# Kernel tuning notes

Measured on AMD Instinct MI355X. Metric: run time of the kernel, lower is better.

## Reference

```python
import jax, jax.numpy as jnp
import numpy as np

D_EMBED = 384
D_FF = 64
TAU = 0.1
T0, T1 = 0.0, 1.0
N_STEPS = 10


def setup_inputs() -> dict:
    key = jax.random.key(0)
    ks = jax.random.split(key, 6)
    B, n, d, f = 64, 1024, D_EMBED, D_FF
    init = lambda k, sh, fan: (jax.random.normal(k, sh, jnp.float32) / np.sqrt(fan)).astype(jnp.float32)
    return {
        "embeddings": jax.random.normal(ks[0], (B, n, d), jnp.float32),
        "W1": init(ks[1], (d + 1, f), d + 1), "b1": jnp.zeros((f,), jnp.float32),
        "W2": init(ks[2], (f, f), f),       "b2": jnp.zeros((f,), jnp.float32),
        "W3": init(ks[3], (f, d), f),       "b3": jnp.zeros((d,), jnp.float32),
        "Ws": init(ks[4], (d, 1), d),       "bs": jnp.zeros((1,), jnp.float32),
    }


def reference(embeddings, W1, b1, W2, b2, W3, b3, Ws, bs):
    B, n, d = embeddings.shape
    h0 = embeddings.reshape(B * n, d)
    dt = (T1 - T0) / N_STEPS

    def ode_f(t, h):
        # time-aware dynamics: concat scalar t to hidden state
        t_col = jnp.full((h.shape[0], 1), t, dtype=h.dtype)
        x = jnp.concatenate([h, t_col], axis=-1)
        x = jnp.tanh(x @ W1 + b1)
        x = jnp.tanh(x @ W2 + b2)
        return x @ W3 + b3

    def rk4_step(h, t):
        k1 = ode_f(t, h)
        k2 = ode_f(t + dt * 0.5, h + (dt * 0.5) * k1)
        k3 = ode_f(t + dt * 0.5, h + (dt * 0.5) * k2)
        k4 = ode_f(t + dt, h + dt * k3)
        return h + (dt / 6.0) * (k1 + 2.0 * k2 + 2.0 * k3 + k4), None

    ts = T0 + dt * jnp.arange(N_STEPS, dtype=jnp.float32)
    h_final, _ = jax.lax.scan(rk4_step, h0, ts)
    h_final = h_final.reshape(B, n, d)

    scores = (h_final @ Ws + bs).squeeze(-1)  # (B, n)

    # NeuralSort (Grover et al.): P_hat = softmax((C - A@1@1^T)^T / tau)
    s_col = scores[:, :, None]                        # (B, n, 1)
    A = jnp.abs(s_col - scores[:, None, :])           # (B, n, n) pairwise |s_i - s_j|
    row_sum = jnp.sum(A, axis=-1, keepdims=True)      # A @ one one^T, broadcast over cols
    scaling = (n + 1 - 2.0 * (jnp.arange(n, dtype=scores.dtype) + 1.0))  # (n,)
    C = s_col * scaling[None, None, :]                # C[b,i,j] = s_i * scaling_j
    P_max = jnp.transpose(C - row_sum, (0, 2, 1))
    P_hat = jax.nn.softmax(P_max / TAU, axis=-1)      # (B, n, n) soft permutation

    x_sorted = jnp.einsum('bij,bjd->bid', P_hat, embeddings)
    return x_sorted, scores
```

## Files before the change

kernel.cpp:

```cpp
#include <hip/hip_runtime.h>
#include <hip/hip_bf16.h>

#define NT 1024
#define DD 384
#define FF 64

typedef __attribute__((ext_vector_type(8))) _Float16 half8;
typedef __attribute__((ext_vector_type(4))) float f32x4;
typedef __attribute__((ext_vector_type(4))) unsigned uint32x4;

#define LO_SCALE 2048.f
#define INV2048  4.8828125e-4f

__device__ __forceinline__ float tanh_fast(float x){
    x = fminf(fmaxf(x, -15.f), 15.f);
    float e = __expf(2.f*x);
    return (e - 1.f) * __builtin_amdgcn_rcpf(e + 1.f);
}

__device__ __forceinline__ unsigned short h2u(_Float16 h){ return __builtin_bit_cast(unsigned short, h); }

__device__ __forceinline__ unsigned short split2_comp(float x, int comp){
    _Float16 hi = (_Float16)x;
    if (comp == 0) return h2u(hi);
    float r = (x - (float)hi) * LO_SCALE;
    _Float16 lo = (_Float16)r;
    return h2u(lo);
}

__device__ __forceinline__ void split_pack4(const float* v, unsigned* ph, unsigned* pl){
#pragma unroll
    for (int p=0;p<2;++p){
        float a=v[2*p], b=v[2*p+1];
        _Float16 ha=(_Float16)a, hb=(_Float16)b;
        ph[p] = (unsigned)h2u(ha) | ((unsigned)h2u(hb)<<16);
        float ra=(a-(float)ha)*LO_SCALE, rb=(b-(float)hb)*LO_SCALE;
        pl[p] = __builtin_bit_cast(unsigned, __builtin_amdgcn_cvt_pkrtz(ra, rb));
    }
}

__global__ void k_prep(const float* __restrict__ W1, const float* __restrict__ W2,
                       const float* __restrict__ W3, unsigned short* __restrict__ F)
{
    unsigned short* W1F = F;
    unsigned short* W2F = F + 49152;
    unsigned short* W3F = F + 57344;
    const int t = blockIdx.x*256 + threadIdx.x;
    const int NTH = gridDim.x*256;
    for (int i=t; i<49152; i+=NTH){
        int j=i&7, l=(i>>3)&63, u=i>>9;
        int kb=u%12, v=u/12, mb=v&3, comp=v>>2;
        int k=kb*32+8*(l>>4)+j, c=mb*16+(l&15);
        W1F[i] = split2_comp(W1[k*64+c], comp);
    }
    for (int i=t; i<8192; i+=NTH){
        int j=i&7, l=(i>>3)&63, u=i>>9;
        int kb=u&1, v=u>>1, mb=v&3, comp=v>>2;
        int k=kb*32+8*(l>>4)+j, c=mb*16+(l&15);
        W2F[i] = split2_comp(W2[k*64+c], comp);
    }
    for (int i=t; i<49152; i+=NTH){
        int j=i&7, l=(i>>3)&63, u=i>>9;
        int kb=u&1, v=u>>1, mb=v%24, comp=v/24;
        int k=kb*32+8*(l>>4)+j, c=mb*16+(l&15);
        W3F[i] = split2_comp(W3[k*384+c], comp);
    }
}

__global__ void k_prepE(const float* __restrict__ emb, unsigned short* __restrict__ EF)
{
    __shared__ float tile[32][388];
    const int b   = blockIdx.x >> 5;
    const int kb  = blockIdx.x & 31;
    const int tid = threadIdx.x;
    const float* src = emb + ((long long)b*NT + kb*32)*DD;
    for (int o = tid; o < 32*96; o += 256){
        int r = o/96, c4 = (o%96)*4;
        *(float4*)&tile[r][c4] = *(const float4*)&src[r*384 + c4];
    }
    __syncthreads();
    unsigned short* dst = EF + ((long long)b*24*32 + kb)*512;
    for (int o = tid; o < 24*512; o += 256){
        int mb = o >> 9, q = o & 511;
        int l = q >> 3, jj = q & 7;
        float v = tile[8*(l>>4)+jj][mb*16 + (l&15)];
        dst[(long long)mb*16384 + q] = h2u((_Float16)v);
    }
}

#define MFMA3(AH,AL,BH,BL,ACC,ACC2) do{ \
    ACC  = __builtin_amdgcn_mfma_f32_16x16x32_f16(AH,BH,ACC,0,0,0); \
    ACC2 = __builtin_amdgcn_mfma_f32_16x16x32_f16(AH,BL,ACC2,0,0,0); \
    ACC2 = __builtin_amdgcn_mfma_f32_16x16x32_f16(AL,BH,ACC2,0,0,0); \
}while(0)

struct AF { half8 h, l; };
#define LDA(P, CS) AF{ *(const half8*)(P), *(const half8*)((P)+(CS)) }
#define LDB(BASE, KB) do{ \
    bh = *(const half8*)((BASE) + (KB)*2048); \
    bl = *(const half8*)((BASE) + (KB)*2048 + 1024); \
}while(0)

__global__ __launch_bounds__(512) __attribute__((amdgpu_waves_per_eu(2,2)))
void k_ode(const float* __restrict__ emb,
           const float* __restrict__ W1,
           const float* __restrict__ b1, const float* __restrict__ b2,
           const float* __restrict__ b3, const float* __restrict__ Ws,
           const float* __restrict__ bs,
           const unsigned short* __restrict__ W1F,
           const unsigned short* __restrict__ W2F,
           const unsigned short* __restrict__ W3F,
           float* __restrict__ scores)
{
    extern __shared__ char smem[];
    unsigned short* hf  = (unsigned short*)smem;
    unsigned short* x1f = hf  + 24576;
    unsigned short* x2f = x1f + 4096;
    unsigned short* w1h = x2f + 4096;
    float*          h0l = (float*)(smem + 114688);

    unsigned* hf32  = (unsigned*)hf;
    unsigned* x1f32 = (unsigned*)x1f;
    unsigned* x2f32 = (unsigned*)x2f;

    const int tid  = threadIdx.x;
    const int lane = tid & 63;
    const int w    = __builtin_amdgcn_readfirstlane(tid >> 6);
    const int g    = lane >> 4;
    const int rr   = lane & 15;
    const int nb   = w & 1;
    const int mbA  = w >> 1;
    const int rowl = nb*16 + rr;
    const long long row0 = (long long)blockIdx.x * 32;
    const float dt = 0.1f;

    {
        const unsigned* srcw = (const unsigned*)W1F;
        unsigned* dstw = (unsigned*)w1h;
        for (int o = tid; o < 12288; o += 512) dstw[o] = srcw[o];
    }

    const unsigned short* hrd  = hf  + nb*512 + lane*8;
    const unsigned short* x1rd = x1f + nb*512 + lane*8;
    const unsigned short* x2rd = x2f + nb*512 + lane*8;
    const unsigned wxp = nb*256 + rr*4 + 2*(g&1);
    const unsigned wx1 = ((unsigned)(mbA>>1))*1024 + 64u*((2*mbA+(g>>1))&3) + wxp;
    const int h0base = rowl*324 + mbA*80 + 4*g;
    float h0r5[4];

    float arc[24];
#pragma unroll
    for (int t=0;t<6;++t){
        f32x4 v = *(const f32x4*)(emb + (row0+rowl)*DD + mbA*96 + t*16 + 4*g);
        float hw[4] = {v[0],v[1],v[2],v[3]};
        if (t < 5) *(float4*)(h0l + h0base + 16*t) = make_float4(hw[0],hw[1],hw[2],hw[3]);
        else {
#pragma unroll
            for (int r=0;r<4;++r) h0r5[r] = hw[r];
        }
        unsigned ph[2],pl[2];
        split_pack4(hw,ph,pl);
        const unsigned wh = ((unsigned)((6*mbA+t)>>1))*1024 + 64u*((2*t+(g>>1))&3) + wxp;
        *(uint2*)(hf32 + wh       ) = make_uint2(ph[0],ph[1]);
        *(uint2*)(hf32 + wh +  512) = make_uint2(pl[0],pl[1]);
    }

#define M3SEC(T, ACC, ACC2) do{ \
    ACC = *(const f32x4*)(b3 + mbA*96 + 16*(T) + 4*g); \
    ACC2 = (f32x4){0.f,0.f,0.f,0.f}; \
    const unsigned short* A3 = W3F + (unsigned)((6*mbA+(T))*2)*512 + lane*8; \
    AF w0 = LDA(A3, 24576); \
    AF w1 = LDA(A3+512, 24576); \
    MFMA3(w0.h,w0.l,B0h,B0l,ACC,ACC2); \
    MFMA3(w1.h,w1.l,B1h,B1l,ACC,ACC2); \
    __builtin_amdgcn_sched_barrier(0); \
}while(0)

#define M3UPD(T, ACC, ACC2) do{ \
    float h0v[4]; \
    if ((T) < 5){ \
        f32x4 _hv = *(const f32x4*)(h0l + h0base + 16*(T)); \
        h0v[0]=_hv[0]; h0v[1]=_hv[1]; h0v[2]=_hv[2]; h0v[3]=_hv[3]; \
    } else { \
        _Pragma("unroll") \
        for (int r=0;r<4;++r) h0v[r] = h0r5[r]; \
    } \
    float hw[4]; \
    if (stage < 3){ \
        _Pragma("unroll") \
        for (int r=0;r<4;++r){ float kr=fmaf(ACC2[r], INV2048, ACC[r]); \
            arc[4*(T)+r] = fmaf(wacc, kr, arc[4*(T)+r]); \
            hw[r] = fmaf(cs, kr, h0v[r]); } \
    } else { \
        _Pragma("unroll") \
        for (int r=0;r<4;++r){ float kr=fmaf(ACC2[r], INV2048, ACC[r]); \
            arc[4*(T)+r] = fmaf(wacc, kr, arc[4*(T)+r]); \
            hw[r] = h0v[r] + arc[4*(T)+r]; } \
        if ((T) < 5) *(float4*)(h0l + h0base + 16*(T)) = make_float4(hw[0],hw[1],hw[2],hw[3]); \
        else { \
            _Pragma("unroll") \
            for (int r=0;r<4;++r) h0r5[r] = hw[r]; \
        } \
    } \
    unsigned ph[2],pl[2]; \
    split_pack4(hw,ph,pl); \
    const unsigned wh = ((unsigned)((6*mbA+(T))>>1))*1024 + 64u*((2*(T)+(g>>1))&3) + wxp; \
    *(uint2*)(hf32 + wh       ) = make_uint2(ph[0],ph[1]); \
    *(uint2*)(hf32 + wh +  512) = make_uint2(pl[0],pl[1]); \
}while(0)

#pragma unroll 1
    for (int step=0; step<10; ++step){
        const float tstep = dt*(float)step;
#pragma unroll
        for (int j=0;j<24;++j) arc[j]=0.f;

#pragma unroll 1
        for (int stage=0; stage<4; ++stage){
            const float ts = tstep + ((stage==0)?0.f:((stage==3)?dt:0.5f*dt));
            __syncthreads();

            f32x4 accA, accB, accLA, accLB;
            {
                f32x4 b1v = *(const f32x4*)(b1 + mbA*16 + 4*g);
                f32x4 wtv = *(const f32x4*)(W1 + 384*64 + mbA*16 + 4*g);
#pragma unroll
                for (int r=0;r<4;++r){ accA[r] = fmaf(ts, wtv[r], b1v[r]); accB[r] = 0.f; accLA[r] = 0.f; accLB[r] = 0.f; }
            }
            {
                const unsigned short* H1 = w1h + mbA*6144 + lane*8;
                const unsigned short* L1 = W1F + 24576 + mbA*6144 + lane*8;
                half8 l0 = *(const half8*)(L1);
                half8 l1 = *(const half8*)(L1 + 512);
#pragma unroll 1
                for (int p=0;p<6;++p){
                    half8 hh0 = *(const half8*)(H1 + (2*p)*512);
                    half8 hh1 = *(const half8*)(H1 + (2*p+1)*512);
                    const int kb2 = (p<5) ? (2*p+2) : 0;
                    half8 nl0 = *(const half8*)(L1 + kb2*512);
                    half8 nl1 = *(const half8*)(L1 + (kb2+1)*512);
                    half8 bh,bl;
                    LDB(hrd, 2*p);
                    MFMA3(hh0,l0,bh,bl,accA,accLA);
                    LDB(hrd, 2*p+1);
                    MFMA3(hh1,l1,bh,bl,accB,accLB);
                    l0 = nl0; l1 = nl1;
                }
            }
            {
                float xv[4];
#pragma unroll
                for (int r=0;r<4;++r) xv[r] = tanh_fast(accA[r] + accB[r] + (accLA[r]+accLB[r])*INV2048);
                unsigned ph[2],pl[2];
                split_pack4(xv,ph,pl);
                *(uint2*)(x1f32 + wx1       ) = make_uint2(ph[0],ph[1]);
                *(uint2*)(x1f32 + wx1 +  512) = make_uint2(pl[0],pl[1]);
            }
            __syncthreads();

            f32x4 acc2 = *(const f32x4*)(b2 + mbA*16 + 4*g);
            f32x4 acc2L;
            {
#pragma unroll
                for (int r=0;r<4;++r) acc2L[r] = 0.f;
                const unsigned short* A2 = W2F + mbA*1024 + lane*8;
                AF c0 = LDA(A2, 4096);
                AF c1 = LDA(A2 + 512, 4096);
                half8 bh,bl;
                LDB(x1rd, 0);
                MFMA3(c0.h,c0.l,bh,bl,acc2,acc2L);
                LDB(x1rd, 1);
                MFMA3(c1.h,c1.l,bh,bl,acc2,acc2L);
            }
            {
                float xv[4];
#pragma unroll
                for (int r=0;r<4;++r) xv[r] = tanh_fast(acc2[r] + acc2L[r]*INV2048);
                unsigned ph[2],pl[2];
                split_pack4(xv,ph,pl);
                *(uint2*)(x2f32 + wx1       ) = make_uint2(ph[0],ph[1]);
                *(uint2*)(x2f32 + wx1 +  512) = make_uint2(pl[0],pl[1]);
            }
            __syncthreads();

            const float wacc = (dt/6.f)*((stage==1||stage==2)?2.f:1.f);
            const float cs   = (stage==2)?dt:0.5f*dt;
            {
                half8 B0h = *(const half8*)(x2rd);
                half8 B0l = *(const half8*)(x2rd + 1024);
                half8 B1h = *(const half8*)(x2rd + 2048);
                half8 B1l = *(const half8*)(x2rd + 3072);
                f32x4 ac0,ac1,ac2b,ac3,ac4,ac5;
                f32x4 c0,c1,c2,c3,c4,c5;
                M3SEC(0, ac0, c0);
                M3SEC(1, ac1, c1);   M3UPD(0, ac0, c0);
                M3SEC(2, ac2b, c2);  M3UPD(1, ac1, c1);
                M3SEC(3, ac3, c3);   M3UPD(2, ac2b, c2);
                M3SEC(4, ac4, c4);   M3UPD(3, ac3, c3);
                M3SEC(5, ac5, c5);   M3UPD(4, ac4, c4);
                M3UPD(5, ac5, c5);
            }
        }
    }

    float part = 0.f;
#pragma unroll
    for (int t=0;t<6;++t){
        float hv[4];
        if (t < 5){
            f32x4 _hv = *(const f32x4*)(h0l + h0base + 16*t);
            hv[0]=_hv[0]; hv[1]=_hv[1]; hv[2]=_hv[2]; hv[3]=_hv[3];
        } else {
#pragma unroll
            for (int r=0;r<4;++r) hv[r] = h0r5[r];
        }
        f32x4 wsv = *(const f32x4*)(Ws + mbA*96 + t*16 + 4*g);
#pragma unroll
        for (int r=0;r<4;++r) part = fmaf(hv[r], wsv[r], part);
    }
    __syncthreads();
    float* red = (float*)x1f;
    red[rowl*16 + mbA*4 + g] = part;
    __syncthreads();
    if (tid < 32){
        float s = bs[0];
#pragma unroll
        for (int q=0;q<16;++q) s += red[tid*16+q];
        scores[row0 + tid] = s;
    }
#undef M3SEC
#undef M3UPD
}

__global__ void k_rowsum(const float* __restrict__ scores, float* __restrict__ rs)
{
    __shared__ float s[NT];
    const int b   = blockIdx.x >> 2;
    const int q   = blockIdx.x & 3;
    const int tid = threadIdx.x;
    for (int i=tid; i<NT; i+=256) s[i] = scores[b*NT + i];
    __syncthreads();
    const int i = q*256 + tid;
    const float si = s[i];
    float sum = 0.f;
#pragma unroll 8
    for (int j=0; j<NT; ++j) sum += fabsf(si - s[j]);
    rs[b*NT + i] = sum;
}

__global__ __launch_bounds__(512)
void k_pvm(const unsigned short* __restrict__ EF, const float* __restrict__ scores,
           const float* __restrict__ rs, float* __restrict__ out)
{
    __shared__ float s_tr[2*NT];
    __shared__ float red_m[16][33];
    __shared__ float red_s[16][33];
    __shared__ float s_MI[64];

    const int tid = threadIdx.x;
    const int b   = blockIdx.x >> 5;
    const int j0  = (blockIdx.x & 31) * 32;
    const float invT2 = 10.f * 1.44269504f;

    for (int i = tid; i < NT; i += 512){
        s_tr[2*i  ] =  scores[b*NT + i] * invT2;
        s_tr[2*i+1] = -rs[b*NT + i] * invT2;
    }
    __syncthreads();

    {
        const int jl = tid & 31;
        const int ch = tid >> 5;
        const float SC = 1023.f - 2.f*(float)(j0 + jl);
        const int ib = ch*64;
        float m = -3.0e38f;
#pragma unroll 4
        for (int i = ib; i < ib+64; ++i)
            m = fmaxf(m, fmaf(s_tr[2*i], SC, s_tr[2*i+1]));
        float sum = 0.f;
#pragma unroll 4
        for (int i = ib; i < ib+64; ++i)
            sum += exp2f(fmaf(s_tr[2*i], SC, s_tr[2*i+1]) - m);
        red_m[ch][jl] = m; red_s[ch][jl] = sum;
    }
    __syncthreads();
    if (tid < 32){
        float M = -3.0e38f;
#pragma unroll
        for (int c=0;c<16;++c) M = fmaxf(M, red_m[c][tid]);
        float S = 0.f;
#pragma unroll
        for (int c=0;c<16;++c) S += red_s[c][tid] * exp2f(red_m[c][tid] - M);
        s_MI[tid]    = M;
        s_MI[32+tid] = __builtin_amdgcn_rcpf(S);
    }
    __syncthreads();

    const int lane = tid & 63;
    const int w    = __builtin_amdgcn_readfirstlane(tid >> 6);
    const int g    = lane >> 4;
    const int rr   = lane & 15;
    const int nb   = w & 1;
    const int mbA  = w >> 1;
    const int jl   = nb*16 + rr;
    const float SCv = 1023.f - 2.f*(float)(j0 + jl);
    const float Mv  = s_MI[jl];
    const float Iv  = s_MI[32 + jl];

    f32x4 ac0={0,0,0,0}, ac1={0,0,0,0}, ac2={0,0,0,0},
          ac3={0,0,0,0}, ac4={0,0,0,0}, ac5={0,0,0,0};

    const unsigned short* Abase = EF + (((long long)b*24 + mbA*6)*32)*512 + lane*8;

#pragma unroll 2
    for (int kb = 0; kb < 32; ++kb){
        const float* str = s_tr + 2*(kb*32 + 8*g);
        uint32x4 pw;
#pragma unroll
        for (int p=0;p<4;++p){
            float L0 = fmaf(str[4*p  ], SCv, str[4*p+1]) - Mv;
            float L1 = fmaf(str[4*p+2], SCv, str[4*p+3]) - Mv;
            pw[p] = __builtin_bit_cast(unsigned,
                        __builtin_amdgcn_cvt_pkrtz(exp2f(L0), exp2f(L1)));
        }
        half8 Pf = __builtin_bit_cast(half8, pw);
        const unsigned short* A = Abase + kb*512;
        ac0 = __builtin_amdgcn_mfma_f32_16x16x32_f16(*(const half8*)(A          ), Pf, ac0, 0,0,0);
        ac1 = __builtin_amdgcn_mfma_f32_16x16x32_f16(*(const half8*)(A + 16384  ), Pf, ac1, 0,0,0);
        ac2 = __builtin_amdgcn_mfma_f32_16x16x32_f16(*(const half8*)(A + 2*16384), Pf, ac2, 0,0,0);
        ac3 = __builtin_amdgcn_mfma_f32_16x16x32_f16(*(const half8*)(A + 3*16384), Pf, ac3, 0,0,0);
        ac4 = __builtin_amdgcn_mfma_f32_16x16x32_f16(*(const half8*)(A + 4*16384), Pf, ac4, 0,0,0);
        ac5 = __builtin_amdgcn_mfma_f32_16x16x32_f16(*(const half8*)(A + 5*16384), Pf, ac5, 0,0,0);
    }

    float* op = out + ((long long)b*NT + j0 + jl)*DD + mbA*96 + 4*g;
    *(float4*)(op       ) = make_float4(ac0[0]*Iv, ac0[1]*Iv, ac0[2]*Iv, ac0[3]*Iv);
    *(float4*)(op + 16  ) = make_float4(ac1[0]*Iv, ac1[1]*Iv, ac1[2]*Iv, ac1[3]*Iv);
    *(float4*)(op + 32  ) = make_float4(ac2[0]*Iv, ac2[1]*Iv, ac2[2]*Iv, ac2[3]*Iv);
    *(float4*)(op + 48  ) = make_float4(ac3[0]*Iv, ac3[1]*Iv, ac3[2]*Iv, ac3[3]*Iv);
    *(float4*)(op + 64  ) = make_float4(ac4[0]*Iv, ac4[1]*Iv, ac4[2]*Iv, ac4[3]*Iv);
    *(float4*)(op + 80  ) = make_float4(ac5[0]*Iv, ac5[1]*Iv, ac5[2]*Iv, ac5[3]*Iv);
}

__global__ __launch_bounds__(256, 2)
void k_pv(const float* __restrict__ emb, const float* __restrict__ scores,
          const float* __restrict__ rs, float* __restrict__ out)
{
    __shared__ float s_tt[NT];
    __shared__ float s_rp[NT];
    __shared__ float red_m[8][33];
    __shared__ float red_s[8][33];
    __shared__ float s_M[32], s_I[32];

    const int tid = threadIdx.x;
    const int b   = blockIdx.x >> 5;
    const int j0  = (blockIdx.x & 31) * 32;
    const float invT = 10.f;

    for (int i=tid; i<NT; i+=256){
        s_tt[i] =  scores[b*NT + i] * invT;
        s_rp[i] = -rs[b*NT + i] * invT;
    }
    __syncthreads();
    {
        const int jl = tid & 31;
        const int ch = tid >> 5;
        const float SC = 1023.f - 2.f*(float)(j0 + jl);
        const int ibeg = ch*128;
        float m = -3.0e38f;
#pragma unroll 4
        for (int i=ibeg; i<ibeg+128; ++i){
            float L = fmaf(s_tt[i], SC, s_rp[i]);
            m = fmaxf(m, L);
        }
        float sum = 0.f;
#pragma unroll 4
        for (int i=ibeg; i<ibeg+128; ++i){
            float L = fmaf(s_tt[i], SC, s_rp[i]);
            sum += __expf(L - m);
        }
        red_m[ch][jl] = m; red_s[ch][jl] = sum;
    }
    __syncthreads();
    if (tid < 32){
        float M = -3.0e38f;
#pragma unroll
        for (int c=0; c<8; ++c) M = fmaxf(M, red_m[c][tid]);
        float S = 0.f;
#pragma unroll
        for (int c=0; c<8; ++c) S += red_s[c][tid]*__expf(red_m[c][tid]-M);
        s_M[tid] = M;
        s_I[tid] = 1.f/S;
    }
    __syncthreads();

    const int tx = tid & 31;
    const int jy = tid >> 5;
    float accv[4][12];
#pragma unroll
    for (int v=0; v<4; ++v)
#pragma unroll
        for (int u=0; u<12; ++u) accv[v][u] = 0.f;

    float SCv[4], Mv[4], Iv[4];
#pragma unroll
    for (int v=0; v<4; ++v){
        const int jl = jy + 8*v;
        SCv[v] = 1023.f - 2.f*(float)(j0 + jl);
        Mv[v]  = s_M[jl];
        Iv[v]  = s_I[jl];
    }
    const float* ep = emb + ((long long)b*NT)*DD + tx;
#pragma unroll 2
    for (int i=0; i<NT; ++i){
        const float ti = s_tt[i], ri = s_rp[i];
        float ev[12];
#pragma unroll
        for (int u=0; u<12; ++u) ev[u] = ep[(long long)i*DD + 32*u];
        float p[4];
#pragma unroll
        for (int v=0; v<4; ++v)
            p[v] = __expf(fmaf(ti, SCv[v], ri) - Mv[v]);
#pragma unroll
        for (int v=0; v<4; ++v)
#pragma unroll
            for (int u=0; u<12; ++u) accv[v][u] = fmaf(p[v], ev[u], accv[v][u]);
    }
#pragma unroll
    for (int v=0; v<4; ++v){
        float* op = out + ((long long)b*NT + j0 + jy + 8*v)*DD + tx;
#pragma unroll
        for (int u=0; u<12; ++u) op[32*u] = accv[v][u]*Iv[v];
    }
}

extern "C" void kernel_launch(void* const* d_in, const int* in_sizes, int n_in,
                              void* d_out, int out_size, void* d_ws, size_t ws_size,
                              hipStream_t stream)
{
    const float* emb = (const float*)d_in[0];
    const float* W1  = (const float*)d_in[1];
    const float* b1  = (const float*)d_in[2];
    const float* W2  = (const float*)d_in[3];
    const float* b2  = (const float*)d_in[4];
    const float* W3  = (const float*)d_in[5];
    const float* b3  = (const float*)d_in[6];
    const float* Ws  = (const float*)d_in[7];
    const float* bs  = (const float*)d_in[8];

    const int B = in_sizes[0] / (NT*DD);
    float* out    = (float*)d_out;
    float* scores = out + (long long)B*NT*DD;

    unsigned short* WF = (unsigned short*)d_ws;
    const unsigned short* W1F = WF;
    const unsigned short* W2F = WF + 49152;
    const unsigned short* W3F = WF + 57344;
    float* rsum = (float*)((char*)d_ws + 319488);

    const size_t efOff = 589824;
    const size_t efBytes = (size_t)B*24*32*512*2;
    const bool useMFMApv = (ws_size >= efOff + efBytes);
    unsigned short* EF = (unsigned short*)((char*)d_ws + efOff);

    const int ODE_LDS = 156160;
    hipFuncSetAttribute(reinterpret_cast<const void*>(k_ode),
                        hipFuncAttributeMaxDynamicSharedMemorySize, ODE_LDS);

    hipLaunchKernelGGL(k_prep, dim3(64), dim3(256), 0, stream, W1, W2, W3, WF);
    if (useMFMApv)
        hipLaunchKernelGGL(k_prepE, dim3(B*32), dim3(256), 0, stream, emb, EF);
    hipLaunchKernelGGL(k_ode, dim3(B*NT/32), dim3(512), ODE_LDS, stream,
                       emb, W1, b1, b2, b3, Ws, bs, W1F, W2F, W3F, scores);
    hipLaunchKernelGGL(k_rowsum, dim3(B*4), dim3(256), 0, stream, scores, rsum);
    if (useMFMApv)
        hipLaunchKernelGGL(k_pvm, dim3(B*32), dim3(512), 0, stream, EF, scores, rsum, out);
    else
        hipLaunchKernelGGL(k_pv, dim3(B*32), dim3(256), 0, stream, emb, scores, rsum, out);
}
```

Measured before the change: 1.322 ms.

## Move ODE state to global scratch and stage W3 hi-parts in LDS

The fp32 ODE state previously held in LDS (h0l) now lives in a global scratch buffer, reusing the output buffer before the final PV kernel overwrites it. Reads are prefetched one section ahead. The freed LDS holds the high-half fp16 W3 fragments for 5 of 6 sections, so those MFMA operands come from LDS instead of global/L2. This trades LDS-resident state for global round trips each stage, which rely on cache hits, in exchange for cheaper W3 operand loads.

Result: slower. 1.370 ms (+3.6%).

```diff
diff --git a/kernel.cpp b/kernel.cpp
--- a/kernel.cpp
+++ b/kernel.cpp
@@ -110,14 +110,15 @@
            const unsigned short* __restrict__ W1F,
            const unsigned short* __restrict__ W2F,
            const unsigned short* __restrict__ W3F,
-           float* __restrict__ scores)
+           float* __restrict__ scores,
+           float* __restrict__ hst)
 {
     extern __shared__ char smem[];
     unsigned short* hf  = (unsigned short*)smem;
     unsigned short* x1f = hf  + 24576;
     unsigned short* x2f = x1f + 4096;
     unsigned short* w1h = x2f + 4096;
-    float*          h0l = (float*)(smem + 114688);
+    unsigned short* w3h = w1h + 24576;
 
     unsigned* hf32  = (unsigned*)hf;
     unsigned* x1f32 = (unsigned*)x1f;
@@ -135,9 +136,16 @@
     const float dt = 0.1f;
 
     {
-        const unsigned* srcw = (const unsigned*)W1F;
-        unsigned* dstw = (unsigned*)w1h;
-        for (int o = tid; o < 12288; o += 512) dstw[o] = srcw[o];
+        const unsigned* s1 = (const unsigned*)W1F;
+        unsigned* d1 = (unsigned*)w1h;
+        for (int o = tid; o < 12288; o += 512) d1[o] = s1[o];
+        const unsigned* s3 = (const unsigned*)W3F;
+        unsigned* d3 = (unsigned*)w3h;
+        for (int o = tid; o < 10240; o += 512){
+            int mbL = o >> 9, q = o & 511;
+            int mbS = (mbL/5)*6 + (mbL - (mbL/5)*5);
+            d3[o] = s3[mbS*512 + q];
+        }
     }
 
     const unsigned short* hrd  = hf  + nb*512 + lane*8;
@@ -145,19 +153,14 @@
     const unsigned short* x2rd = x2f + nb*512 + lane*8;
     const unsigned wxp = nb*256 + rr*4 + 2*(g&1);
     const unsigned wx1 = ((unsigned)(mbA>>1))*1024 + 64u*((2*mbA+(g>>1))&3) + wxp;
-    const int h0base = rowl*324 + mbA*80 + 4*g;
-    float h0r5[4];
+    const unsigned hoff = (unsigned)blockIdx.x*12288u + (unsigned)tid*4u;
 
     float arc[24];
 #pragma unroll
     for (int t=0;t<6;++t){
         f32x4 v = *(const f32x4*)(emb + (row0+rowl)*DD + mbA*96 + t*16 + 4*g);
         float hw[4] = {v[0],v[1],v[2],v[3]};
-        if (t < 5) *(float4*)(h0l + h0base + 16*t) = make_float4(hw[0],hw[1],hw[2],hw[3]);
-        else {
-#pragma unroll
-            for (int r=0;r<4;++r) h0r5[r] = hw[r];
-        }
+        *(float4*)(hst + hoff + 2048u*t) = make_float4(hw[0],hw[1],hw[2],hw[3]);
         unsigned ph[2],pl[2];
         split_pack4(hw,ph,pl);
         const unsigned wh = ((unsigned)((6*mbA+t)>>1))*1024 + 64u*((2*t+(g>>1))&3) + wxp;
@@ -168,39 +171,35 @@
 #define M3SEC(T, ACC, ACC2) do{ \
     ACC = *(const f32x4*)(b3 + mbA*96 + 16*(T) + 4*g); \
     ACC2 = (f32x4){0.f,0.f,0.f,0.f}; \
-    const unsigned short* A3 = W3F + (unsigned)((6*mbA+(T))*2)*512 + lane*8; \
-    AF w0 = LDA(A3, 24576); \
-    AF w1 = LDA(A3+512, 24576); \
-    MFMA3(w0.h,w0.l,B0h,B0l,ACC,ACC2); \
-    MFMA3(w1.h,w1.l,B1h,B1l,ACC,ACC2); \
+    half8 w0h_, w0l_, w1h_, w1l_; \
+    if ((T) < 5){ \
+        const unsigned short* AH = w3h + (unsigned)((5*mbA+(T))*2)*512 + lane*8; \
+        const unsigned short* AL = W3F + 24576 + (unsigned)((6*mbA+(T))*2)*512 + lane*8; \
+        w0h_ = *(const half8*)(AH);        w0l_ = *(const half8*)(AL); \
+        w1h_ = *(const half8*)(AH + 512);  w1l_ = *(const half8*)(AL + 512); \
+    } else { \
+        const unsigned short* A3 = W3F + (unsigned)((6*mbA+(T))*2)*512 + lane*8; \
+        w0h_ = *(const half8*)(A3);          w0l_ = *(const half8*)(A3 + 24576); \
+        w1h_ = *(const half8*)(A3 + 512);    w1l_ = *(const half8*)(A3 + 24576 + 512); \
+    } \
+    MFMA3(w0h_,w0l_,B0h,B0l,ACC,ACC2); \
+    MFMA3(w1h_,w1l_,B1h,B1l,ACC,ACC2); \
     __builtin_amdgcn_sched_barrier(0); \
 }while(0)
 
-#define M3UPD(T, ACC, ACC2) do{ \
-    float h0v[4]; \
-    if ((T) < 5){ \
-        f32x4 _hv = *(const f32x4*)(h0l + h0base + 16*(T)); \
-        h0v[0]=_hv[0]; h0v[1]=_hv[1]; h0v[2]=_hv[2]; h0v[3]=_hv[3]; \
-    } else { \
-        _Pragma("unroll") \
-        for (int r=0;r<4;++r) h0v[r] = h0r5[r]; \
-    } \
+#define M3UPD(T, ACC, ACC2, H0V) do{ \
     float hw[4]; \
     if (stage < 3){ \
         _Pragma("unroll") \
         for (int r=0;r<4;++r){ float kr=fmaf(ACC2[r], INV2048, ACC[r]); \
             arc[4*(T)+r] = fmaf(wacc, kr, arc[4*(T)+r]); \
-            hw[r] = fmaf(cs, kr, h0v[r]); } \
+            hw[r] = fmaf(cs, kr, H0V[r]); } \
     } else { \
         _Pragma("unroll") \
         for (int r=0;r<4;++r){ float kr=fmaf(ACC2[r], INV2048, ACC[r]); \
             arc[4*(T)+r] = fmaf(wacc, kr, arc[4*(T)+r]); \
-            hw[r] = h0v[r] + arc[4*(T)+r]; } \
-        if ((T) < 5) *(float4*)(h0l + h0base + 16*(T)) = make_float4(hw[0],hw[1],hw[2],hw[3]); \
-        else { \
-            _Pragma("unroll") \
-            for (int r=0;r<4;++r) h0r5[r] = hw[r]; \
-        } \
+            hw[r] = H0V[r] + arc[4*(T)+r]; } \
+        *(float4*)(hst + hoff + 2048u*(T)) = make_float4(hw[0],hw[1],hw[2],hw[3]); \
     } \
     unsigned ph[2],pl[2]; \
     split_pack4(hw,ph,pl); \
@@ -292,13 +291,19 @@
                 half8 B1l = *(const half8*)(x2rd + 3072);
                 f32x4 ac0,ac1,ac2b,ac3,ac4,ac5;
                 f32x4 c0,c1,c2,c3,c4,c5;
+                f32x4 hpA = *(const f32x4*)(hst + hoff);
+                f32x4 hpB = *(const f32x4*)(hst + hoff + 2048u);
                 M3SEC(0, ac0, c0);
-                M3SEC(1, ac1, c1);   M3UPD(0, ac0, c0);
-                M3SEC(2, ac2b, c2);  M3UPD(1, ac1, c1);
-                M3SEC(3, ac3, c3);   M3UPD(2, ac2b, c2);
-                M3SEC(4, ac4, c4);   M3UPD(3, ac3, c3);
-                M3SEC(5, ac5, c5);   M3UPD(4, ac4, c4);
-                M3UPD(5, ac5, c5);
+                M3SEC(1, ac1, c1);   M3UPD(0, ac0, c0, hpA);
+                hpA = *(const f32x4*)(hst + hoff + 2048u*2);
+                M3SEC(2, ac2b, c2);  M3UPD(1, ac1, c1, hpB);
+                hpB = *(const f32x4*)(hst + hoff + 2048u*3);
+                M3SEC(3, ac3, c3);   M3UPD(2, ac2b, c2, hpA);
+                hpA = *(const f32x4*)(hst + hoff + 2048u*4);
+                M3SEC(4, ac4, c4);   M3UPD(3, ac3, c3, hpB);
+                hpB = *(const f32x4*)(hst + hoff + 2048u*5);
+                M3SEC(5, ac5, c5);   M3UPD(4, ac4, c4, hpA);
+                M3UPD(5, ac5, c5, hpB);
             }
         }
     }
@@ -306,14 +311,7 @@
     float part = 0.f;
 #pragma unroll
     for (int t=0;t<6;++t){
-        float hv[4];
-        if (t < 5){
-            f32x4 _hv = *(const f32x4*)(h0l + h0base + 16*t);
-            hv[0]=_hv[0]; hv[1]=_hv[1]; hv[2]=_hv[2]; hv[3]=_hv[3];
-        } else {
-#pragma unroll
-            for (int r=0;r<4;++r) hv[r] = h0r5[r];
-        }
+        f32x4 hv  = *(const f32x4*)(hst + hoff + 2048u*t);
         f32x4 wsv = *(const f32x4*)(Ws + mbA*96 + t*16 + 4*g);
 #pragma unroll
         for (int r=0;r<4;++r) part = fmaf(hv[r], wsv[r], part);
@@ -563,7 +561,7 @@
     const bool useMFMApv = (ws_size >= efOff + efBytes);
     unsigned short* EF = (unsigned short*)((char*)d_ws + efOff);
 
-    const int ODE_LDS = 156160;
+    const int ODE_LDS = 155648;
     hipFuncSetAttribute(reinterpret_cast<const void*>(k_ode),
                         hipFuncAttributeMaxDynamicSharedMemorySize, ODE_LDS);
 
@@ -571,7 +569,7 @@
     if (useMFMApv)
         hipLaunchKernelGGL(k_prepE, dim3(B*32), dim3(256), 0, stream, emb, EF);
     hipLaunchKernelGGL(k_ode, dim3(B*NT/32), dim3(512), ODE_LDS, stream,
-                       emb, W1, b1, b2, b3, Ws, bs, W1F, W2F, W3F, scores);
+                       emb, W1, b1, b2, b3, Ws, bs, W1F, W2F, W3F, scores, out);
     hipLaunchKernelGGL(k_rowsum, dim3(B*4), dim3(256), 0, stream, scores, rsum);
     if (useMFMApv)
         hipLaunchKernelGGL(k_pvm, dim3(B*32), dim3(512), 0, stream, EF, scores, rsum, out);
```
